# Kernel tuning notes

Hardware: AMD Instinct MI355X
Metric: run time of the kernel (lower is better)

## Reference

```python
import jax, jax.numpy as jnp
import numpy as np

MARGIN = 1.0  # init kwarg 'margin'
N, D = 8192, 128
NUM_CLASSES = 100

def setup_inputs() -> dict:
    key = jax.random.key(0)
    kx, ky = jax.random.split(key)
    x = jax.random.normal(kx, (N, D), dtype=jnp.float32)
    y = jax.random.randint(ky, (N,), 0, NUM_CLASSES, dtype=jnp.int64)
    return {"x": x, "y": y}

def reference(x, y):
    # Squared euclidean pairwise distances: d[i,j] = sum_k (x[i,k] - x[j,k])^2
    # computed via the ||a||^2 + ||b||^2 - 2 a.b expansion to avoid an NxNxD
    # intermediate. Clamp tiny negatives from fp roundoff.
    sq = jnp.sum(x * x, axis=-1)                      # [N]
    d = sq[:, None] + sq[None, :] - 2.0 * (x @ x.T)   # [N, N]
    d = jnp.maximum(d, 0.0)
    same = (y[:, None] == y[None, :]).astype(x.dtype)  # [N, N] positive-pair mask
    # Faithful to the torch module: dissimilar pairs contribute d, similar
    # pairs contribute hinge clamp(margin - d, 0); mean over all N*N pairs.
    loss = jnp.mean((1.0 - same) * d + same * jnp.maximum(MARGIN - d, 0.0))
    return loss
```

## Files before the change

kernel.cpp:

```cpp
#include <hip/hip_runtime.h>


#define N_ROWS 8192
#define DIM    128
#define NCLS   100
#define MARGINV 1.0
#define CAP    224
#define LDSTRIDE 136
#define K1_BLOCKS 128
#define K1_ROWS  (N_ROWS / K1_BLOCKS)
#define NT2 512

typedef _Float16 half8 __attribute__((ext_vector_type(8)));
typedef _Float16 half4v __attribute__((ext_vector_type(4)));
typedef float   float4v __attribute__((ext_vector_type(4)));

__global__ __launch_bounds__(256) void scan_kernel(
    const float* __restrict__ x, const int* __restrict__ y,
    float* __restrict__ colpart, float* __restrict__ sqpart,
    float* __restrict__ sqm_g, int* __restrict__ cnt, int* __restrict__ list)
{
    const int b = blockIdx.x, tid = threadIdx.x;
    const int l = tid & 31, g = tid >> 5;
    const int base = b * K1_ROWS;
    const float4* x4 = (const float4*)x;
    float4 ca = make_float4(0.f, 0.f, 0.f, 0.f);
    __shared__ float  sqred[K1_ROWS];
    __shared__ float4 colred[256];

    #pragma unroll
    for (int pass = 0; pass < K1_ROWS / 8; ++pass) {
        int r = base + pass * 8 + g;
        float4 v = x4[r * 32 + l];
        ca.x += v.x; ca.y += v.y; ca.z += v.z; ca.w += v.w;
        float s = v.x*v.x + v.y*v.y + v.z*v.z + v.w*v.w;
        s += __shfl_xor(s, 1); s += __shfl_xor(s, 2); s += __shfl_xor(s, 4);
        s += __shfl_xor(s, 8); s += __shfl_xor(s, 16);
        if (l == 0) {
            sqm_g[r] = s;
            sqred[pass * 8 + g] = s;
            int c = y[r];
            int p = atomicAdd(&cnt[c], 1);
            if (p < CAP) list[c * CAP + p] = r;
        }
    }
    colred[tid] = ca;
    __syncthreads();
    if (tid < 32) {
        float4 a = colred[tid];
        #pragma unroll
        for (int gg = 1; gg < 8; ++gg) {
            float4 t = colred[tid + 32 * gg];
            a.x += t.x; a.y += t.y; a.z += t.z; a.w += t.w;
        }
        ((float4*)colpart)[b * 32 + tid] = a;
        float s2 = sqred[tid] + sqred[tid + 32];
        s2 += __shfl_xor(s2, 1); s2 += __shfl_xor(s2, 2); s2 += __shfl_xor(s2, 4);
        s2 += __shfl_xor(s2, 8); s2 += __shfl_xor(s2, 16);
        if (tid == 0) sqpart[b] = s2;
    }
}

__global__ __launch_bounds__(NT2) void gram_kernel(
    const float* __restrict__ x, const float* __restrict__ sqm_g,
    const int* __restrict__ cnt, const int* __restrict__ list,
    float* __restrict__ SSc, float* __restrict__ NSQc, float* __restrict__ Hc)
{
    const int c = blockIdx.x, tid = threadIdx.x;
    __shared__ __align__(16) _Float16 xh[CAP * LDSTRIDE];
    __shared__ int   llist[CAP];
    __shared__ float sqm[CAP];
    __shared__ float4 colred[NT2];
    __shared__ float  red[NT2];

    const int mtrue = cnt[c];
    const int m = mtrue < CAP ? mtrue : CAP;
    if (tid < m) llist[tid] = list[c * CAP + tid];
    __syncthreads();
    const int ntiles = (m + 15) >> 4;
    const int mpad   = ntiles << 4;

    const float4* x4 = (const float4*)x;
    const int q4 = tid & 31;
    float4 ca = make_float4(0.f, 0.f, 0.f, 0.f);
    for (int k = tid >> 5; k < m; k += NT2 / 32) {
        float4 v = x4[llist[k] * 32 + q4];
        ca.x += v.x; ca.y += v.y; ca.z += v.z; ca.w += v.w;
        half4v h;
        h[0] = (_Float16)v.x; h[1] = (_Float16)v.y;
        h[2] = (_Float16)v.z; h[3] = (_Float16)v.w;
        *(half4v*)(xh + k * LDSTRIDE + q4 * 4) = h;
    }
    for (int j = tid; j < (mpad - m) * DIM; j += NT2) {
        int rr = m + (j >> 7), d = j & 127;
        xh[rr * LDSTRIDE + d] = (_Float16)0.f;
    }
    float sv = 0.f;
    if (tid < m)        { sv = sqm_g[llist[tid]]; sqm[tid] = sv; }
    else if (tid < mpad){ sqm[tid] = 0.f; }
    colred[tid] = ca;
    red[tid] = sv;
    __syncthreads();

    if (tid < 32) {
        float4 S = colred[tid];
        #pragma unroll
        for (int gg = 1; gg < NT2 / 32; ++gg) {
            float4 t = colred[tid + 32 * gg];
            S.x += t.x; S.y += t.y; S.z += t.z; S.w += t.w;
        }
        float ss = S.x*S.x + S.y*S.y + S.z*S.z + S.w*S.w;
        ss += __shfl_xor(ss, 1); ss += __shfl_xor(ss, 2); ss += __shfl_xor(ss, 4);
        ss += __shfl_xor(ss, 8); ss += __shfl_xor(ss, 16);
        if (tid == 0) SSc[c] = ss;
    }
    for (int s = NT2 / 2; s > 0; s >>= 1) {
        __syncthreads();
        if (tid < s) red[tid] += red[tid + s];
    }
    __syncthreads();
    if (tid == 0) NSQc[c] = (float)mtrue * red[0];

    float hacc = 0.f;
    {
        const int wave = tid >> 6, lane = tid & 63;
        const int lr = lane & 15, q = lane >> 4;
        const int ntp = ntiles * (ntiles + 1) / 2;
        for (int tp = wave; tp < ntp; tp += NT2 / 64) {
            int ta = 0, rem = tp;
            while (rem >= ntiles - ta) { rem -= ntiles - ta; ++ta; }
            int tb = ta + rem;
            const half8* arow = (const half8*)(xh + (ta * 16 + lr) * LDSTRIDE + q * 8);
            const half8* brow = (const half8*)(xh + (tb * 16 + lr) * LDSTRIDE + q * 8);
            float4v acc = {0.f, 0.f, 0.f, 0.f};
            #pragma unroll
            for (int kb = 0; kb < 4; ++kb)
                acc = __builtin_amdgcn_mfma_f32_16x16x32_f16(arow[kb * 4], brow[kb * 4], acc, 0, 0, 0);
            float w = (ta == tb) ? 1.f : 2.f;
            #pragma unroll
            for (int i = 0; i < 4; ++i) {
                int a  = ta * 16 + q * 4 + i;
                int bb = tb * 16 + lr;
                if (a < m && bb < m && a != bb) {
                    float d = sqm[a] + sqm[bb] - 2.f * acc[i];
                    d = fmaxf(d, 0.f);
                    hacc += w * fmaxf((float)MARGINV - d, 0.f);
                }
            }
        }
    }
    __syncthreads();
    red[tid] = hacc;
    for (int s = NT2 / 2; s > 0; s >>= 1) {
        __syncthreads();
        if (tid < s) red[tid] += red[tid + s];
    }
    __syncthreads();
    if (tid == 0) Hc[c] = red[0];
}

__global__ __launch_bounds__(256) void final_kernel(
    const float* __restrict__ colpart, const float* __restrict__ sqpart,
    const float* __restrict__ SSc, const float* __restrict__ NSQc,
    const float* __restrict__ Hc, float* __restrict__ out)
{
    const int tid = threadIdx.x;
    __shared__ double dred[256];
    __shared__ float  Scol[DIM];
    {
        const int d = tid & 127, h = tid >> 7;
        float s = 0.f;
        for (int b = h; b < K1_BLOCKS; b += 2) s += colpart[b * DIM + d];
        if (h == 1) Scol[d] = s;
        __syncthreads();
        if (h == 0) Scol[d] += s;
        __syncthreads();
    }
    double ns = (tid < DIM)       ? (double)Scol[tid] * (double)Scol[tid] : 0.0;
    double sq = (tid < K1_BLOCKS) ? (double)sqpart[tid] : 0.0;
    double ss = 0.0, nsq = 0.0, hg = 0.0;
    if (tid < NCLS) { ss = SSc[tid]; nsq = NSQc[tid]; hg = Hc[tid]; }

    auto br = [&](double v) -> double {
        dred[tid] = v; __syncthreads();
        for (int s = 128; s > 0; s >>= 1) {
            if (tid < s) dred[tid] += dred[tid + s];
            __syncthreads();
        }
        double r = dred[0]; __syncthreads(); return r;
    };
    double NS = br(ns), SQ = br(sq), SS = br(ss), NSQ = br(nsq), H = br(hg);
    if (tid == 0) {
        const double Nf = (double)N_ROWS;
        double sum_all  = 2.0 * Nf * SQ - 2.0 * NS;
        double sum_same = 2.0 * NSQ - 2.0 * SS;
        double total    = (sum_all - sum_same) + Nf * (double)MARGINV + H;
        out[0] = (float)(total / (Nf * Nf));
    }
}

extern "C" void kernel_launch(void* const* d_in, const int* in_sizes, int n_in,
                              void* d_out, int out_size, void* d_ws, size_t ws_size,
                              hipStream_t stream) {
    const float* x = (const float*)d_in[0];
    const int*   y = (const int*)d_in[1];

    float* colpart = (float*)d_ws;
    float* sqpart  = colpart + K1_BLOCKS * DIM;
    float* sqm_g   = sqpart + K1_BLOCKS;
    float* SSc     = sqm_g + N_ROWS;
    float* NSQc    = SSc + NCLS;
    float* Hc      = NSQc + NCLS;
    int*   cnt     = (int*)(Hc + NCLS);
    int*   list    = cnt + NCLS;

    hipMemsetAsync(cnt, 0, NCLS * sizeof(int), stream);
    scan_kernel <<<K1_BLOCKS, 256, 0, stream>>>(x, y, colpart, sqpart, sqm_g, cnt, list);
    gram_kernel <<<NCLS, NT2, 0, stream>>>(x, sqm_g, cnt, list, SSc, NSQc, Hc);
    final_kernel<<<1, 256, 0, stream>>>(colpart, sqpart, SSc, NSQc, Hc, (float*)d_out);
}
```

Before: 108.4 us.

## Scatter fp16 rows by class in scan and fuse final reduction into gram

The scan kernel now writes each row as fp16 directly into a per-class bucket in global memory, along with its squared norm. The gram kernel then reads those buckets with MFMA straight from global memory instead of gathering and staging through LDS. The per-class sum-squared term is obtained from the dot products instead of a column reduction, and the final kernel is folded into the gram kernel through a last-block atomic counter. This removes a launch and the LDS staging, and the scan grid is doubled. The cost is unstaged, uncoalesced global fragment loads in the MFMA loop and a larger workspace.

After: 124.3 us. +14.7%, slower.

```diff
diff --git a/kernel.cpp b/kernel.cpp
--- a/kernel.cpp
+++ b/kernel.cpp
@@ -4,45 +4,46 @@
 #define N_ROWS 8192
 #define DIM    128
 #define NCLS   100
-#define MARGINV 1.0
 #define CAP    224
-#define LDSTRIDE 136
-#define K1_BLOCKS 128
-#define K1_ROWS  (N_ROWS / K1_BLOCKS)
-#define NT2 512
+#define SB     256
+#define SROWS  (N_ROWS / SB)
 
-typedef _Float16 half8 __attribute__((ext_vector_type(8)));
+typedef _Float16 half8  __attribute__((ext_vector_type(8)));
 typedef _Float16 half4v __attribute__((ext_vector_type(4)));
-typedef float   float4v __attribute__((ext_vector_type(4)));
+typedef float    float4v __attribute__((ext_vector_type(4)));
 
 __global__ __launch_bounds__(256) void scan_kernel(
     const float* __restrict__ x, const int* __restrict__ y,
-    float* __restrict__ colpart, float* __restrict__ sqpart,
-    float* __restrict__ sqm_g, int* __restrict__ cnt, int* __restrict__ list)
+    _Float16* __restrict__ gh, float* __restrict__ sqg, int* __restrict__ cnt,
+    float* __restrict__ colpart, float* __restrict__ sqpart)
 {
     const int b = blockIdx.x, tid = threadIdx.x;
     const int l = tid & 31, g = tid >> 5;
-    const int base = b * K1_ROWS;
     const float4* x4 = (const float4*)x;
     float4 ca = make_float4(0.f, 0.f, 0.f, 0.f);
-    __shared__ float  sqred[K1_ROWS];
+    __shared__ float  sqred[SROWS];
     __shared__ float4 colred[256];
 
     #pragma unroll
-    for (int pass = 0; pass < K1_ROWS / 8; ++pass) {
-        int r = base + pass * 8 + g;
+    for (int pass = 0; pass < SROWS / 8; ++pass) {
+        const int r = b * SROWS + pass * 8 + g;
         float4 v = x4[r * 32 + l];
         ca.x += v.x; ca.y += v.y; ca.z += v.z; ca.w += v.w;
         float s = v.x*v.x + v.y*v.y + v.z*v.z + v.w*v.w;
-        s += __shfl_xor(s, 1); s += __shfl_xor(s, 2); s += __shfl_xor(s, 4);
-        s += __shfl_xor(s, 8); s += __shfl_xor(s, 16);
-        if (l == 0) {
-            sqm_g[r] = s;
-            sqred[pass * 8 + g] = s;
-            int c = y[r];
-            int p = atomicAdd(&cnt[c], 1);
-            if (p < CAP) list[c * CAP + p] = r;
+        s += __shfl_xor(s, 1);  s += __shfl_xor(s, 2);  s += __shfl_xor(s, 4);
+        s += __shfl_xor(s, 8);  s += __shfl_xor(s, 16);
+        const int c = y[r];
+        int p = 0;
+        if (l == 0) p = atomicAdd(&cnt[c], 1);
+        p = __shfl(p, 0, 32);
+        if (p < CAP) {
+            half4v h;
+            h[0] = (_Float16)v.x; h[1] = (_Float16)v.y;
+            h[2] = (_Float16)v.z; h[3] = (_Float16)v.w;
+            *(half4v*)(gh + (size_t)(c * CAP + p) * DIM + l * 4) = h;
+            if (l == 0) sqg[c * CAP + p] = s;
         }
+        if (l == 0) sqred[pass * 8 + g] = s;
     }
     colred[tid] = ca;
     __syncthreads();
@@ -54,149 +55,124 @@
             a.x += t.x; a.y += t.y; a.z += t.z; a.w += t.w;
         }
         ((float4*)colpart)[b * 32 + tid] = a;
-        float s2 = sqred[tid] + sqred[tid + 32];
-        s2 += __shfl_xor(s2, 1); s2 += __shfl_xor(s2, 2); s2 += __shfl_xor(s2, 4);
-        s2 += __shfl_xor(s2, 8); s2 += __shfl_xor(s2, 16);
+        float s2 = sqred[tid];
+        s2 += __shfl_xor(s2, 1);  s2 += __shfl_xor(s2, 2);  s2 += __shfl_xor(s2, 4);
+        s2 += __shfl_xor(s2, 8);  s2 += __shfl_xor(s2, 16);
         if (tid == 0) sqpart[b] = s2;
     }
 }
 
-__global__ __launch_bounds__(NT2) void gram_kernel(
-    const float* __restrict__ x, const float* __restrict__ sqm_g,
-    const int* __restrict__ cnt, const int* __restrict__ list,
-    float* __restrict__ SSc, float* __restrict__ NSQc, float* __restrict__ Hc)
+__global__ __launch_bounds__(256) void gram_kernel(
+    const _Float16* __restrict__ gh, const float* __restrict__ sqg,
+    const int* __restrict__ cnt,
+    const float* __restrict__ colpart, const float* __restrict__ sqpart,
+    float* __restrict__ Hc, float* __restrict__ SSc, float* __restrict__ NSQc,
+    int* __restrict__ done, float* __restrict__ out)
 {
     const int c = blockIdx.x, tid = threadIdx.x;
-    __shared__ __align__(16) _Float16 xh[CAP * LDSTRIDE];
-    __shared__ int   llist[CAP];
     __shared__ float sqm[CAP];
-    __shared__ float4 colred[NT2];
-    __shared__ float  red[NT2];
+    __shared__ float wred[8];
+    __shared__ float qred[4];
+    __shared__ int   lastFlag;
 
     const int mtrue = cnt[c];
     const int m = mtrue < CAP ? mtrue : CAP;
-    if (tid < m) llist[tid] = list[c * CAP + tid];
-    __syncthreads();
     const int ntiles = (m + 15) >> 4;
-    const int mpad   = ntiles << 4;
 
-    const float4* x4 = (const float4*)x;
-    const int q4 = tid & 31;
-    float4 ca = make_float4(0.f, 0.f, 0.f, 0.f);
-    for (int k = tid >> 5; k < m; k += NT2 / 32) {
-        float4 v = x4[llist[k] * 32 + q4];
-        ca.x += v.x; ca.y += v.y; ca.z += v.z; ca.w += v.w;
-        half4v h;
-        h[0] = (_Float16)v.x; h[1] = (_Float16)v.y;
-        h[2] = (_Float16)v.z; h[3] = (_Float16)v.w;
-        *(half4v*)(xh + k * LDSTRIDE + q4 * 4) = h;
+    if (tid < CAP) sqm[tid] = (tid < m) ? sqg[c * CAP + tid] : 0.f;
+    float q0 = (tid < m) ? sqg[c * CAP + tid] : 0.f;
+
+    const int wave = tid >> 6, lane = tid & 63;
+    const int lr = lane & 15, q = lane >> 4;
+    {
+        #pragma unroll
+        for (int off = 32; off > 0; off >>= 1) q0 += __shfl_xor(q0, off);
+        if (lane == 0) qred[wave] = q0;
     }
-    for (int j = tid; j < (mpad - m) * DIM; j += NT2) {
-        int rr = m + (j >> 7), d = j & 127;
-        xh[rr * LDSTRIDE + d] = (_Float16)0.f;
-    }
-    float sv = 0.f;
-    if (tid < m)        { sv = sqm_g[llist[tid]]; sqm[tid] = sv; }
-    else if (tid < mpad){ sqm[tid] = 0.f; }
-    colred[tid] = ca;
-    red[tid] = sv;
     __syncthreads();
 
-    if (tid < 32) {
-        float4 S = colred[tid];
-        #pragma unroll
-        for (int gg = 1; gg < NT2 / 32; ++gg) {
-            float4 t = colred[tid + 32 * gg];
-            S.x += t.x; S.y += t.y; S.z += t.z; S.w += t.w;
-        }
-        float ss = S.x*S.x + S.y*S.y + S.z*S.z + S.w*S.w;
-        ss += __shfl_xor(ss, 1); ss += __shfl_xor(ss, 2); ss += __shfl_xor(ss, 4);
-        ss += __shfl_xor(ss, 8); ss += __shfl_xor(ss, 16);
-        if (tid == 0) SSc[c] = ss;
-    }
-    for (int s = NT2 / 2; s > 0; s >>= 1) {
-        __syncthreads();
-        if (tid < s) red[tid] += red[tid + s];
-    }
-    __syncthreads();
-    if (tid == 0) NSQc[c] = (float)mtrue * red[0];
-
-    float hacc = 0.f;
+    float hacc = 0.f, dsum = 0.f;
     {
-        const int wave = tid >> 6, lane = tid & 63;
-        const int lr = lane & 15, q = lane >> 4;
+        const _Float16* base = gh + (size_t)c * CAP * DIM;
         const int ntp = ntiles * (ntiles + 1) / 2;
-        for (int tp = wave; tp < ntp; tp += NT2 / 64) {
+        const half8 z = {0, 0, 0, 0, 0, 0, 0, 0};
+        for (int tp = wave; tp < ntp; tp += 4) {
             int ta = 0, rem = tp;
             while (rem >= ntiles - ta) { rem -= ntiles - ta; ++ta; }
-            int tb = ta + rem;
-            const half8* arow = (const half8*)(xh + (ta * 16 + lr) * LDSTRIDE + q * 8);
-            const half8* brow = (const half8*)(xh + (tb * 16 + lr) * LDSTRIDE + q * 8);
+            const int tb = ta + rem;
+            const int ra = ta * 16 + lr, rb = tb * 16 + lr;
+            const half8* ap = (const half8*)(base + ra * DIM + q * 8);
+            const half8* bp = (const half8*)(base + rb * DIM + q * 8);
+            const bool va = ra < m, vb = rb < m;
             float4v acc = {0.f, 0.f, 0.f, 0.f};
             #pragma unroll
-            for (int kb = 0; kb < 4; ++kb)
-                acc = __builtin_amdgcn_mfma_f32_16x16x32_f16(arow[kb * 4], brow[kb * 4], acc, 0, 0, 0);
-            float w = (ta == tb) ? 1.f : 2.f;
+            for (int kb = 0; kb < 4; ++kb) {
+                half8 af = va ? ap[kb * 4] : z;
+                half8 bf = vb ? bp[kb * 4] : z;
+                acc = __builtin_amdgcn_mfma_f32_16x16x32_f16(af, bf, acc, 0, 0, 0);
+            }
+            const float w = (ta == tb) ? 1.f : 2.f;
             #pragma unroll
             for (int i = 0; i < 4; ++i) {
-                int a  = ta * 16 + q * 4 + i;
-                int bb = tb * 16 + lr;
-                if (a < m && bb < m && a != bb) {
-                    float d = sqm[a] + sqm[bb] - 2.f * acc[i];
-                    d = fmaxf(d, 0.f);
-                    hacc += w * fmaxf((float)MARGINV - d, 0.f);
+                const int a  = ta * 16 + q * 4 + i;
+                const int bb = tb * 16 + lr;
+                if (a < m && bb < m) {
+                    const float dot = acc[i];
+                    dsum += w * dot;
+                    if (a != bb) {
+                        float d = fmaxf(sqm[a] + sqm[bb] - 2.f * dot, 0.f);
+                        hacc += w * fmaxf(1.f - d, 0.f);
+                    }
                 }
             }
         }
     }
+    #pragma unroll
+    for (int off = 32; off > 0; off >>= 1) {
+        hacc += __shfl_xor(hacc, off);
+        dsum += __shfl_xor(dsum, off);
+    }
+    if (lane == 0) { wred[wave] = hacc; wred[4 + wave] = dsum; }
     __syncthreads();
-    red[tid] = hacc;
-    for (int s = NT2 / 2; s > 0; s >>= 1) {
-        __syncthreads();
-        if (tid < s) red[tid] += red[tid + s];
+    if (tid == 0) {
+        Hc[c]   = wred[0] + wred[1] + wred[2] + wred[3];
+        SSc[c]  = wred[4] + wred[5] + wred[6] + wred[7];
+        NSQc[c] = (float)mtrue * (qred[0] + qred[1] + qred[2] + qred[3]);
+        __threadfence();
+        int p = atomicAdd(done, 1);
+        lastFlag = (p == NCLS - 1);
     }
     __syncthreads();
-    if (tid == 0) Hc[c] = red[0];
-}
+    if (!lastFlag) return;
 
-__global__ __launch_bounds__(256) void final_kernel(
-    const float* __restrict__ colpart, const float* __restrict__ sqpart,
-    const float* __restrict__ SSc, const float* __restrict__ NSQc,
-    const float* __restrict__ Hc, float* __restrict__ out)
-{
-    const int tid = threadIdx.x;
+    __threadfence();
+    __shared__ float  scol[DIM];
     __shared__ double dred[256];
-    __shared__ float  Scol[DIM];
     {
         const int d = tid & 127, h = tid >> 7;
         float s = 0.f;
-        for (int b = h; b < K1_BLOCKS; b += 2) s += colpart[b * DIM + d];
-        if (h == 1) Scol[d] = s;
+        for (int b = h; b < SB; b += 2) s += colpart[b * DIM + d];
+        if (h == 0) scol[d] = s;
         __syncthreads();
-        if (h == 0) Scol[d] += s;
+        if (h == 1) scol[d] += s;
         __syncthreads();
     }
-    double ns = (tid < DIM)       ? (double)Scol[tid] * (double)Scol[tid] : 0.0;
-    double sq = (tid < K1_BLOCKS) ? (double)sqpart[tid] : 0.0;
-    double ss = 0.0, nsq = 0.0, hg = 0.0;
-    if (tid < NCLS) { ss = SSc[tid]; nsq = NSQc[tid]; hg = Hc[tid]; }
-
-    auto br = [&](double v) -> double {
-        dred[tid] = v; __syncthreads();
-        for (int s = 128; s > 0; s >>= 1) {
-            if (tid < s) dred[tid] += dred[tid + s];
-            __syncthreads();
-        }
-        double r = dred[0]; __syncthreads(); return r;
-    };
-    double NS = br(ns), SQ = br(sq), SS = br(ss), NSQ = br(nsq), H = br(hg);
-    if (tid == 0) {
-        const double Nf = (double)N_ROWS;
-        double sum_all  = 2.0 * Nf * SQ - 2.0 * NS;
-        double sum_same = 2.0 * NSQ - 2.0 * SS;
-        double total    = (sum_all - sum_same) + Nf * (double)MARGINV + H;
-        out[0] = (float)(total / (Nf * Nf));
+    const double Nf = (double)N_ROWS;
+    double contrib = 0.0;
+    if (tid < DIM)  { double v = scol[tid]; contrib -= 2.0 * v * v; }
+    contrib += 2.0 * Nf * (double)sqpart[tid];
+    if (tid < NCLS) {
+        contrib -= 2.0 * (double)NSQc[tid];
+        contrib += 2.0 * (double)SSc[tid];
+        contrib += (double)Hc[tid];
     }
+    dred[tid] = contrib;
+    __syncthreads();
+    for (int s = 128; s > 0; s >>= 1) {
+        if (tid < s) dred[tid] += dred[tid + s];
+        __syncthreads();
+    }
+    if (tid == 0) out[0] = (float)((dred[0] + Nf * 1.0 ) / (Nf * Nf));
 }
 
 extern "C" void kernel_launch(void* const* d_in, const int* in_sizes, int n_in,
@@ -205,17 +181,18 @@
     const float* x = (const float*)d_in[0];
     const int*   y = (const int*)d_in[1];
 
-    float* colpart = (float*)d_ws;
-    float* sqpart  = colpart + K1_BLOCKS * DIM;
-    float* sqm_g   = sqpart + K1_BLOCKS;
-    float* SSc     = sqm_g + N_ROWS;
+    _Float16* gh   = (_Float16*)d_ws;
+    float* sqg     = (float*)(gh + (size_t)NCLS * CAP * DIM);
+    float* colpart = sqg + NCLS * CAP;
+    float* sqpart  = colpart + SB * DIM;
+    float* Hc      = sqpart + SB;
+    float* SSc     = Hc + NCLS;
     float* NSQc    = SSc + NCLS;
-    float* Hc      = NSQc + NCLS;
-    int*   cnt     = (int*)(Hc + NCLS);
-    int*   list    = cnt + NCLS;
+    int*   cnt     = (int*)(NSQc + NCLS);
+    int*   done    = cnt + NCLS;
 
-    hipMemsetAsync(cnt, 0, NCLS * sizeof(int), stream);
-    scan_kernel <<<K1_BLOCKS, 256, 0, stream>>>(x, y, colpart, sqpart, sqm_g, cnt, list);
-    gram_kernel <<<NCLS, NT2, 0, stream>>>(x, sqm_g, cnt, list, SSc, NSQc, Hc);
-    final_kernel<<<1, 256, 0, stream>>>(colpart, sqpart, SSc, NSQc, Hc, (float*)d_out);
+    hipMemsetAsync(cnt, 0, (NCLS + 1) * sizeof(int), stream);
+    scan_kernel<<<SB,   256, 0, stream>>>(x, y, gh, sqg, cnt, colpart, sqpart);
+    gram_kernel<<<NCLS, 256, 0, stream>>>(gh, sqg, cnt, colpart, sqpart,
+                                          Hc, SSc, NSQc, done, (float*)d_out);
 }
```
